# Kernel optimization log

Hardware: AMD Instinct MI355X
Metric: run time of the kernel (lower is better)

The kernel has to match this reference:

```python
import jax, jax.numpy as jnp
import numpy as np

BN_EPS = 1e-5
B, N1, N2, C = 4, 16384, 4096, 128
MLP = [256, 256]
IN_CH = 3 * C


def setup_inputs() -> dict:
    key = jax.random.key(0)
    ks = jax.random.split(key, 32)
    inp = {
        "xyz1": jax.random.normal(ks[0], (B, N1, 3), dtype=jnp.float32),
        "xyz2": jax.random.normal(ks[1], (B, N2, 3), dtype=jnp.float32),
        "points2": jax.random.normal(ks[2], (B, C, N2), dtype=jnp.float32),
        "points1": jax.random.normal(ks[3], (B, C, N1), dtype=jnp.float32),
        "points_b1": jax.random.normal(ks[4], (B, C, N1), dtype=jnp.float32),
    }
    ch = IN_CH
    k = 5
    for i, oc in enumerate(MLP):
        inp[f"w{i}"] = jax.random.normal(ks[k], (oc, ch), dtype=jnp.float32) / np.float32(np.sqrt(ch)); k += 1
        inp[f"b{i}"] = jnp.zeros((oc,), dtype=jnp.float32)
        inp[f"g{i}"] = jax.random.uniform(ks[k], (oc,), minval=0.5, maxval=1.5, dtype=jnp.float32); k += 1
        inp[f"beta{i}"] = 0.1 * jax.random.normal(ks[k], (oc,), dtype=jnp.float32); k += 1
        inp[f"m{i}"] = 0.1 * jax.random.normal(ks[k], (oc,), dtype=jnp.float32); k += 1
        inp[f"v{i}"] = jax.random.uniform(ks[k], (oc,), minval=0.5, maxval=1.5, dtype=jnp.float32); k += 1
        ch = oc
    return inp


def _conv_bn_relu(x, w, b, g, beta, m, v):
    # 1x1 conv over channel dim: x (B, Cin, N) -> (B, Cout, N), BN in eval mode, ReLU
    y = jnp.einsum("oc,bcn->bon", w, x) + b[None, :, None]
    y = (y - m[None, :, None]) * jax.lax.rsqrt(v[None, :, None] + BN_EPS) * g[None, :, None] + beta[None, :, None]
    return jax.nn.relu(y)


def reference(xyz1, xyz2, points2, points1, points_b1,
              w0, b0, g0, beta0, m0, v0,
              w1, b1, g1, beta1, m1, v1):
    # squared pairwise distances (B, N1, N2) via GEMM form
    d = (jnp.sum(xyz1 * xyz1, axis=-1)[:, :, None]
         + jnp.sum(xyz2 * xyz2, axis=-1)[:, None, :]
         - 2.0 * jnp.einsum("bnd,bmd->bnm", xyz1, xyz2))
    neg_d3, idx3 = jax.lax.top_k(-d, 3)              # 3 smallest distances
    d3 = -neg_d3                                      # (B, N1, 3)
    w = 1.0 / d3
    w = w / jnp.sum(w, axis=-1, keepdims=True)        # (B, N1, 3)
    p2t = jnp.transpose(points2, (0, 2, 1))           # (B, N2, C)
    gathered = jax.vmap(lambda p, i: p[i])(p2t, idx3) # (B, N1, 3, C)
    fused = jnp.einsum("bnk,bnkc->bcn", w, gathered)  # (B, C, N1)
    x = jnp.concatenate([points1, fused, points_b1], axis=1)  # (B, 3C, N1)
    x = _conv_bn_relu(x, w0, b0, g0, beta0, m0, v0)
    x = _conv_bn_relu(x, w1, b1, g1, beta1, m1, v1)
    return jnp.max(x, axis=1)                         # (B, N1)
```

## Files before the change

### kernel.cpp

```cpp
#include <hip/hip_runtime.h>

#define N1 16384
#define N2 4096
#define CC 128
#define KIN 384
#define HID 256

typedef unsigned short u16;
typedef unsigned int u32;

typedef _Float16 v8h __attribute__((ext_vector_type(8)));
typedef float v4f __attribute__((ext_vector_type(4)));


__device__ __forceinline__ u16 f2h(float f) {
    _Float16 h = (_Float16)f;
    return __builtin_bit_cast(u16, h);
}

__global__ __launch_bounds__(256) void prep_transpose_kernel(
    const float* __restrict__ w0, const float* __restrict__ w1,
    const float* __restrict__ b0, const float* __restrict__ g0, const float* __restrict__ be0,
    const float* __restrict__ m0, const float* __restrict__ v0,
    const float* __restrict__ b1, const float* __restrict__ g1, const float* __restrict__ be1,
    const float* __restrict__ m1, const float* __restrict__ v1,
    const float* __restrict__ xyz2, const float* __restrict__ points2,
    u16* __restrict__ W0h, u16* __restrict__ W1h,
    float* __restrict__ sst, float4* __restrict__ xyz2q,
    float* __restrict__ p2t)
{
    __shared__ float tile[64][129];
    int tid = threadIdx.x;

    if (blockIdx.x < 256) {
        int bid = blockIdx.x;
        int n20 = (bid & 63) * 64;
        int b   = bid >> 6;

        int jr = tid & 63, cr = tid >> 6;
#pragma unroll 8
        for (int it = 0; it < 32; ++it) {
            int ch = it * 4 + cr;
            tile[jr][ch] = points2[((size_t)b * CC + ch) * N2 + n20 + jr];
        }
        __syncthreads();

        int cw = tid & 127, jw0 = tid >> 7;
#pragma unroll 8
        for (int it = 0; it < 32; ++it) {
            int j = it * 2 + jw0;
            p2t[((size_t)b * N2 + n20 + j) * CC + cw] = tile[j][cw];
        }
        return;
    }

    int id = (blockIdx.x - 256) * 256 + tid;
    if (id < 98304) {
        W0h[id] = f2h(w0[id]);
    } else if (id < 163840) {
        int t = id - 98304;
        W1h[t] = f2h(w1[t]);
    } else if (id < 164352) {
        int t = id - 163840;
        int o = t & 255;
        if (t < 256) {
            float s = g0[o] * rsqrtf(v0[o] + 1e-5f);
            sst[o]       = s;
            sst[256 + o] = (b0[o] - m0[o]) * s + be0[o];
        } else {
            float s = g1[o] * rsqrtf(v1[o] + 1e-5f);
            sst[512 + o] = s;
            sst[768 + o] = (b1[o] - m1[o]) * s + be1[o];
        }
    } else if (id < 180736) {
        int t = id - 164352;
        float x = xyz2[(size_t)t * 3 + 0];
        float y = xyz2[(size_t)t * 3 + 1];
        float z = xyz2[(size_t)t * 3 + 2];
        xyz2q[t] = make_float4(x, y, z, fmaf(x, x, fmaf(y, y, z * z)));
    }
}

#define BINS(t, cand, D0, D1, D2, I0, I1, I2) do {                    \
    bool c0 = (t) < (D0);                                             \
    bool c1 = (t) < (D1);                                             \
    bool c2 = (t) < (D2);                                             \
    I2 = c1 ? (I1) : (c2 ? (cand) : (I2));                \
    I1 = c0 ? (I0) : (c1 ? (cand) : (I1));                \
    I0 = c0 ? (cand) : (I0);                                          \
    D2 = __builtin_amdgcn_fmed3f((D1), (t), (D2));        \
    D1 = __builtin_amdgcn_fmed3f((D0), (t), (D1));        \
    D0 = fminf((t), (D0));                                            \
} while (0)

#define INS3LEX(t, j, D0, D1, D2, I0, I1, I2) do {                    \
    bool lt2 = (t) < (D2) || ((t) == (D2) && (j) < (I2));             \
    bool lt1 = (t) < (D1) || ((t) == (D1) && (j) < (I1));             \
    bool lt0 = (t) < (D0) || ((t) == (D0) && (j) < (I0));             \
    if (lt2) {                                                        \
        if (lt1) {                                                    \
            D2 = (D1); I2 = (I1);                                     \
            if (lt0) { D1 = (D0); I1 = (I0); D0 = (t); I0 = (j); }    \
            else     { D1 = (t); I1 = (j); }                          \
        } else { D2 = (t); I2 = (j); }                                \
    }                                                                 \
} while (0)

#define MERGE_STEP(st, D0, D1, D2, I0, I1, I2) do {                   \
    float e0 = __shfl_xor((D0), (st), 64);                            \
    float e1 = __shfl_xor((D1), (st), 64);                            \
    float e2 = __shfl_xor((D2), (st), 64);                            \
    int   j0 = __shfl_xor((I0), (st), 64);                            \
    int   j1 = __shfl_xor((I1), (st), 64);                            \
    int   j2 = __shfl_xor((I2), (st), 64);                            \
    INS3LEX(e0, j0, D0, D1, D2, I0, I1, I2);                          \
    INS3LEX(e1, j1, D0, D1, D2, I0, I1, I2);                          \
    INS3LEX(e2, j2, D0, D1, D2, I0, I1, I2);                          \
} while (0)

#define KNN_OUT(Q, D0, D1, D2, I0, I1, I2, PP) do {                   \
    float r0 = 1.f / ((D0) + (PP));                                   \
    float r1 = 1.f / ((D1) + (PP));                                   \
    float r2 = 1.f / ((D2) + (PP));                                   \
    float inv = 1.f / (r0 + r1 + r2);                                 \
    size_t o3 = ((size_t)b * N1 + p0 + (Q)) * 3;                      \
    idx3[o3]     = (I0);                                              \
    idx3[o3 + 1] = (I1);                                              \
    idx3[o3 + 2] = (I2);                                              \
    w3[o3]     = r0 * inv;                                            \
    w3[o3 + 1] = r1 * inv;                                            \
    w3[o3 + 2] = r2 * inv;                                            \
} while (0)

__global__ __launch_bounds__(256)
__attribute__((amdgpu_waves_per_eu(8, 8)))
void knn_kernel(
    const float* __restrict__ xyz1, const float4* __restrict__ xyz2q,
    int* __restrict__ idx3, float* __restrict__ w3)
{
    __shared__ float4 slds[1024];

    int tid = threadIdx.x;
    int b   = blockIdx.y;
    int n0  = blockIdx.x * 32;

    int s  = tid & 15;
    int g  = tid >> 4;
    int p0 = n0 + g * 2;

    size_t pb = ((size_t)b * N1 + p0) * 3;
    float x0 = xyz1[pb + 0], y0 = xyz1[pb + 1], z0 = xyz1[pb + 2];
    float x1 = xyz1[pb + 3], y1 = xyz1[pb + 4], z1 = xyz1[pb + 5];
    float ax0 = -2.f * x0, ay0 = -2.f * y0, az0 = -2.f * z0;
    float ax1 = -2.f * x1, ay1 = -2.f * y1, az1 = -2.f * z1;
    float pp0 = fmaf(x0, x0, fmaf(y0, y0, z0 * z0));
    float pp1 = fmaf(x1, x1, fmaf(y1, y1, z1 * z1));

    float da0 = 1e30f, da1 = 1e30f, da2 = 1e30f;
    float db0 = 1e30f, db1 = 1e30f, db2 = 1e30f;
    int   ia0 = 0, ia1 = 0, ia2 = 0;
    int   ib0 = 0, ib1 = 0, ib2 = 0;

#pragma unroll
    for (int stage = 0; stage < 4; ++stage) {
        int base = stage * 1024;
#pragma unroll
        for (int i = 0; i < 4; ++i)
            slds[tid + i * 256] = xyz2q[(size_t)b * N2 + base + tid + i * 256];
        __syncthreads();

#pragma unroll 4
        for (int k = 0; k < 64; ++k) {
            int c = s + (k << 4);
            float4 v = slds[c];
            int cand = base + c;
            float t0 = fmaf(ax0, v.x, fmaf(ay0, v.y, fmaf(az0, v.z, v.w)));
            float t1 = fmaf(ax1, v.x, fmaf(ay1, v.y, fmaf(az1, v.z, v.w)));
            BINS(t0, cand, da0, da1, da2, ia0, ia1, ia2);
            BINS(t1, cand, db0, db1, db2, ib0, ib1, ib2);
        }
        __syncthreads();
    }

#pragma unroll
    for (int st = 1; st <= 8; st <<= 1) {
        MERGE_STEP(st, da0, da1, da2, ia0, ia1, ia2);
        MERGE_STEP(st, db0, db1, db2, ib0, ib1, ib2);
    }

    if (s == 0) {
        KNN_OUT(0, da0, da1, da2, ia0, ia1, ia2, pp0);
        KNN_OUT(1, db0, db1, db2, ib0, ib1, ib2, pp1);
    }
}

__global__ __launch_bounds__(256)
__attribute__((amdgpu_waves_per_eu(5, 5)))
void mlp_kernel(
    const float* __restrict__ points1, const float* __restrict__ pointsb1,
    const float4* __restrict__ p2t4,
    const int* __restrict__ idx3, const float* __restrict__ w3,
    const uint4* __restrict__ W0v, const uint4* __restrict__ W1v,
    const float* __restrict__ sst, float* __restrict__ out)
{
    __shared__ __align__(16) u16 sx[32 * KIN];
    __shared__ float sred[4][32];
    __shared__ int   s_idx[96];
    __shared__ float s_w[96];

    int tid = threadIdx.x;
    int b   = blockIdx.y;
    int n0  = blockIdx.x * 32;

    if (tid < 96) {
        size_t gi = ((size_t)b * N1 + n0) * 3 + tid;
        s_idx[tid] = idx3[gi];
        s_w[tid]   = w3[gi];
    }

    int pL = tid & 31;
    int t4 = (tid >> 5) * 4;
#pragma unroll
    for (int k = 0; k < 4; ++k) {
        int r4 = t4 + 32 * k;
        size_t base = ((size_t)b * CC + r4) * N1 + n0 + pL;
        float a0 = points1[base];
        float a1 = points1[base + (size_t)N1];
        float a2 = points1[base + (size_t)2 * N1];
        float a3 = points1[base + (size_t)3 * N1];
        u32 lo = f2h(a0) | ((u32)f2h(a1) << 16);
        u32 hi = f2h(a2) | ((u32)f2h(a3) << 16);
        int chunk = (r4 >> 3) ^ (pL & 7);
        *(uint2*)&sx[pL * KIN + chunk * 8 + (r4 & 7)] = make_uint2(lo, hi);
    }
#pragma unroll
    for (int k = 0; k < 4; ++k) {
        int r4 = t4 + 32 * k;
        int k4 = 256 + r4;
        size_t base = ((size_t)b * CC + r4) * N1 + n0 + pL;
        float a0 = pointsb1[base];
        float a1 = pointsb1[base + (size_t)N1];
        float a2 = pointsb1[base + (size_t)2 * N1];
        float a3 = pointsb1[base + (size_t)3 * N1];
        u32 lo = f2h(a0) | ((u32)f2h(a1) << 16);
        u32 hi = f2h(a2) | ((u32)f2h(a3) << 16);
        int chunk = (k4 >> 3) ^ (pL & 7);
        *(uint2*)&sx[pL * KIN + chunk * 8 + (k4 & 7)] = make_uint2(lo, hi);
    }
    __syncthreads();

    int c4  = tid & 31;
    int pg  = tid >> 5;
    int k4g = 128 + c4 * 4;
#pragma unroll
    for (int k = 0; k < 4; ++k) {
        int p = pg + 8 * k;
        float w0w = s_w[p * 3 + 0], w1w = s_w[p * 3 + 1], w2w = s_w[p * 3 + 2];
        float4 f0 = p2t4[((size_t)b * N2 + s_idx[p * 3 + 0]) * 32 + c4];
        float4 f1 = p2t4[((size_t)b * N2 + s_idx[p * 3 + 1]) * 32 + c4];
        float4 f2 = p2t4[((size_t)b * N2 + s_idx[p * 3 + 2]) * 32 + c4];
        float e0 = fmaf(w0w, f0.x, fmaf(w1w, f1.x, w2w * f2.x));
        float e1 = fmaf(w0w, f0.y, fmaf(w1w, f1.y, w2w * f2.y));
        float e2 = fmaf(w0w, f0.z, fmaf(w1w, f1.z, w2w * f2.z));
        float e3 = fmaf(w0w, f0.w, fmaf(w1w, f1.w, w2w * f2.w));
        u32 lo = f2h(e0) | ((u32)f2h(e1) << 16);
        u32 hi = f2h(e2) | ((u32)f2h(e3) << 16);
        int chunk = (k4g >> 3) ^ (p & 7);
        *(uint2*)&sx[p * KIN + chunk * 8 + (k4g & 7)] = make_uint2(lo, hi);
    }
    __syncthreads();

    int lane = tid & 63, w = tid >> 6;
    int ml = lane & 15, ql = lane >> 4;
    int px7 = ml & 7;

    v4f acc1[4][2];
#pragma unroll
    for (int ot = 0; ot < 4; ++ot)
        for (int pt = 0; pt < 2; ++pt)
            acc1[ot][pt] = (v4f){0.f, 0.f, 0.f, 0.f};

#pragma unroll
    for (int s = 0; s < 12; ++s) {
        int kc = s * 4 + ql;
        int pc = (kc ^ px7) * 8;
        v8h bf0 = __builtin_bit_cast(v8h, *(const uint4*)&sx[ml * KIN + pc]);
        v8h bf1 = __builtin_bit_cast(v8h, *(const uint4*)&sx[(16 + ml) * KIN + pc]);
#pragma unroll
        for (int ot = 0; ot < 4; ++ot) {
            int o = w * 64 + ot * 16 + ml;
            v8h af = __builtin_bit_cast(v8h, W0v[o * 48 + kc]);
            acc1[ot][0] = __builtin_amdgcn_mfma_f32_16x16x32_f16(af, bf0, acc1[ot][0], 0, 0, 0);
            acc1[ot][1] = __builtin_amdgcn_mfma_f32_16x16x32_f16(af, bf1, acc1[ot][1], 0, 0, 0);
        }
    }
    __syncthreads();

    const float* s0v = sst;
    const float* t0v = sst + 256;
#pragma unroll
    for (int ot = 0; ot < 4; ++ot) {
        int o0 = w * 64 + ot * 16 + ql * 4;
        float sc0 = s0v[o0], sc1 = s0v[o0 + 1], sc2 = s0v[o0 + 2], sc3 = s0v[o0 + 3];
        float sh0 = t0v[o0], sh1 = t0v[o0 + 1], sh2 = t0v[o0 + 2], sh3 = t0v[o0 + 3];
        int chunk = ((o0 >> 3) ^ px7);
#pragma unroll
        for (int pt = 0; pt < 2; ++pt) {
            int p = pt * 16 + ml;
            float z0 = fmaxf(fmaf(acc1[ot][pt][0], sc0, sh0), 0.f);
            float z1 = fmaxf(fmaf(acc1[ot][pt][1], sc1, sh1), 0.f);
            float z2 = fmaxf(fmaf(acc1[ot][pt][2], sc2, sh2), 0.f);
            float z3 = fmaxf(fmaf(acc1[ot][pt][3], sc3, sh3), 0.f);
            u32 lo = f2h(z0) | ((u32)f2h(z1) << 16);
            u32 hi = f2h(z2) | ((u32)f2h(z3) << 16);
            *(uint2*)&sx[p * HID + chunk * 8 + (o0 & 7)] = make_uint2(lo, hi);
        }
    }
    __syncthreads();

    v4f acc2[4][2];
#pragma unroll
    for (int ot = 0; ot < 4; ++ot)
        for (int pt = 0; pt < 2; ++pt)
            acc2[ot][pt] = (v4f){0.f, 0.f, 0.f, 0.f};

#pragma unroll
    for (int s = 0; s < 8; ++s) {
        int kc = s * 4 + ql;
        int pc = (kc ^ px7) * 8;
        v8h bf0 = __builtin_bit_cast(v8h, *(const uint4*)&sx[ml * HID + pc]);
        v8h bf1 = __builtin_bit_cast(v8h, *(const uint4*)&sx[(16 + ml) * HID + pc]);
#pragma unroll
        for (int ot = 0; ot < 4; ++ot) {
            int o = w * 64 + ot * 16 + ml;
            v8h af = __builtin_bit_cast(v8h, W1v[o * 32 + kc]);
            acc2[ot][0] = __builtin_amdgcn_mfma_f32_16x16x32_f16(af, bf0, acc2[ot][0], 0, 0, 0);
            acc2[ot][1] = __builtin_amdgcn_mfma_f32_16x16x32_f16(af, bf1, acc2[ot][1], 0, 0, 0);
        }
    }

    const float* s1v = sst + 512;
    const float* t1v = sst + 768;
    float mx0 = 0.f, mx1 = 0.f;
#pragma unroll
    for (int ot = 0; ot < 4; ++ot) {
        int o0 = w * 64 + ot * 16 + ql * 4;
#pragma unroll
        for (int r = 0; r < 4; ++r) {
            float sc = s1v[o0 + r], sh = t1v[o0 + r];
            mx0 = fmaxf(mx0, fmaf(acc2[ot][0][r], sc, sh));
            mx1 = fmaxf(mx1, fmaf(acc2[ot][1][r], sc, sh));
        }
    }
    mx0 = fmaxf(mx0, __shfl_xor(mx0, 16, 64));
    mx0 = fmaxf(mx0, __shfl_xor(mx0, 32, 64));
    mx1 = fmaxf(mx1, __shfl_xor(mx1, 16, 64));
    mx1 = fmaxf(mx1, __shfl_xor(mx1, 32, 64));
    if (lane < 16) {
        sred[w][ml]      = mx0;
        sred[w][16 + ml] = mx1;
    }
    __syncthreads();
    if (tid < 32)
        out[(size_t)b * N1 + n0 + tid] =
            fmaxf(fmaxf(sred[0][tid], sred[1][tid]),
                  fmaxf(sred[2][tid], sred[3][tid]));
}

extern "C" void kernel_launch(void* const* d_in, const int* in_sizes, int n_in,
                              void* d_out, int out_size, void* d_ws, size_t ws_size,
                              hipStream_t stream)
{
    const float* xyz1     = (const float*)d_in[0];
    const float* xyz2     = (const float*)d_in[1];
    const float* points2  = (const float*)d_in[2];
    const float* points1  = (const float*)d_in[3];
    const float* pointsb1 = (const float*)d_in[4];
    const float* w0   = (const float*)d_in[5];
    const float* b0   = (const float*)d_in[6];
    const float* g0   = (const float*)d_in[7];
    const float* be0  = (const float*)d_in[8];
    const float* m0   = (const float*)d_in[9];
    const float* v0   = (const float*)d_in[10];
    const float* w1   = (const float*)d_in[11];
    const float* b1   = (const float*)d_in[12];
    const float* g1   = (const float*)d_in[13];
    const float* be1  = (const float*)d_in[14];
    const float* m1   = (const float*)d_in[15];
    const float* v1   = (const float*)d_in[16];
    float* out = (float*)d_out;

    char* ws = (char*)d_ws;
    u16*    W0h   = (u16*)(ws + 0);
    u16*    W1h   = (u16*)(ws + 196608);
    float*  sst   = (float*)(ws + 327680);
    float4* xyz2q = (float4*)(ws + 331776);
    int*    idx3  = (int*)(ws + 593920);
    float*  w3    = (float*)(ws + 1380352);
    float*  p2t   = (float*)(ws + 2166784);

    prep_transpose_kernel<<<962, 256, 0, stream>>>(
        w0, w1, b0, g0, be0, m0, v0,
        b1, g1, be1, m1, v1,
        xyz2, points2,
        W0h, W1h, sst, xyz2q, p2t);
    knn_kernel<<<dim3(512, 4), 256, 0, stream>>>(xyz1, xyz2q, idx3, w3);
    mlp_kernel<<<dim3(512, 4), 256, 0, stream>>>(points1, pointsb1,
                                                 (const float4*)p2t, idx3, w3,
                                                 (const uint4*)W0h, (const uint4*)W1h,
                                                 sst, out);
}
```

Before: 316.9 us.

## Retile MLP kernel to 64 points per 512-thread block with 8 waves

The MLP kernel now processes 64 points per block using 512 threads (8 waves). Each wave covers 32 output channels across 4 point tiles instead of 64 channels across 2 tiles. This halves the number of blocks and means each weight fragment loaded from global memory feeds four MFMAs instead of two, cutting weight traffic per point. In exchange, LDS use per block doubles to about 48KB, which may limit occupancy, and the fixed waves_per_eu hint is replaced by launch bounds.

After: 279.2 us, median of 2. 11.9% less time.

```diff
diff --git a/kernel.cpp b/kernel.cpp
--- a/kernel.cpp
+++ b/kernel.cpp
@@ -194,8 +194,7 @@
     }
 }
 
-__global__ __launch_bounds__(256)
-__attribute__((amdgpu_waves_per_eu(5, 5)))
+__global__ __launch_bounds__(512, 4)
 void mlp_kernel(
     const float* __restrict__ points1, const float* __restrict__ pointsb1,
     const float4* __restrict__ p2t4,
@@ -203,26 +202,26 @@
     const uint4* __restrict__ W0v, const uint4* __restrict__ W1v,
     const float* __restrict__ sst, float* __restrict__ out)
 {
-    __shared__ __align__(16) u16 sx[32 * KIN];
-    __shared__ float sred[4][32];
-    __shared__ int   s_idx[96];
-    __shared__ float s_w[96];
+    __shared__ __align__(16) u16 sx[64 * KIN];
+    __shared__ float sred[8][64];
+    __shared__ int   s_idx[192];
+    __shared__ float s_w[192];
 
     int tid = threadIdx.x;
     int b   = blockIdx.y;
-    int n0  = blockIdx.x * 32;
-
-    if (tid < 96) {
+    int n0  = blockIdx.x * 64;
+
+    if (tid < 192) {
         size_t gi = ((size_t)b * N1 + n0) * 3 + tid;
         s_idx[tid] = idx3[gi];
         s_w[tid]   = w3[gi];
     }
 
-    int pL = tid & 31;
-    int t4 = (tid >> 5) * 4;
+    int pL  = tid & 63;
+    int cg4 = (tid >> 6) * 4;
 #pragma unroll
     for (int k = 0; k < 4; ++k) {
-        int r4 = t4 + 32 * k;
+        int r4 = cg4 + 32 * k;
         size_t base = ((size_t)b * CC + r4) * N1 + n0 + pL;
         float a0 = points1[base];
         float a1 = points1[base + (size_t)N1];
@@ -235,7 +234,7 @@
     }
 #pragma unroll
     for (int k = 0; k < 4; ++k) {
-        int r4 = t4 + 32 * k;
+        int r4 = cg4 + 32 * k;
         int k4 = 256 + r4;
         size_t base = ((size_t)b * CC + r4) * N1 + n0 + pL;
         float a0 = pointsb1[base];
@@ -254,7 +253,7 @@
     int k4g = 128 + c4 * 4;
 #pragma unroll
     for (int k = 0; k < 4; ++k) {
-        int p = pg + 8 * k;
+        int p = pg + 16 * k;
         float w0w = s_w[p * 3 + 0], w1w = s_w[p * 3 + 1], w2w = s_w[p * 3 + 2];
         float4 f0 = p2t4[((size_t)b * N2 + s_idx[p * 3 + 0]) * 32 + c4];
         float4 f1 = p2t4[((size_t)b * N2 + s_idx[p * 3 + 1]) * 32 + c4];
@@ -274,10 +273,10 @@
     int ml = lane & 15, ql = lane >> 4;
     int px7 = ml & 7;
 
-    v4f acc1[4][2];
-#pragma unroll
-    for (int ot = 0; ot < 4; ++ot)
-        for (int pt = 0; pt < 2; ++pt)
+    v4f acc1[2][4];
+#pragma unroll
+    for (int ot = 0; ot < 2; ++ot)
+        for (int pt = 0; pt < 4; ++pt)
             acc1[ot][pt] = (v4f){0.f, 0.f, 0.f, 0.f};
 
 #pragma unroll
@@ -286,12 +285,16 @@
         int pc = (kc ^ px7) * 8;
         v8h bf0 = __builtin_bit_cast(v8h, *(const uint4*)&sx[ml * KIN + pc]);
         v8h bf1 = __builtin_bit_cast(v8h, *(const uint4*)&sx[(16 + ml) * KIN + pc]);
-#pragma unroll
-        for (int ot = 0; ot < 4; ++ot) {
-            int o = w * 64 + ot * 16 + ml;
+        v8h bf2 = __builtin_bit_cast(v8h, *(const uint4*)&sx[(32 + ml) * KIN + pc]);
+        v8h bf3 = __builtin_bit_cast(v8h, *(const uint4*)&sx[(48 + ml) * KIN + pc]);
+#pragma unroll
+        for (int ot = 0; ot < 2; ++ot) {
+            int o = w * 32 + ot * 16 + ml;
             v8h af = __builtin_bit_cast(v8h, W0v[o * 48 + kc]);
             acc1[ot][0] = __builtin_amdgcn_mfma_f32_16x16x32_f16(af, bf0, acc1[ot][0], 0, 0, 0);
             acc1[ot][1] = __builtin_amdgcn_mfma_f32_16x16x32_f16(af, bf1, acc1[ot][1], 0, 0, 0);
+            acc1[ot][2] = __builtin_amdgcn_mfma_f32_16x16x32_f16(af, bf2, acc1[ot][2], 0, 0, 0);
+            acc1[ot][3] = __builtin_amdgcn_mfma_f32_16x16x32_f16(af, bf3, acc1[ot][3], 0, 0, 0);
         }
     }
     __syncthreads();
@@ -299,13 +302,13 @@
     const float* s0v = sst;
     const float* t0v = sst + 256;
 #pragma unroll
-    for (int ot = 0; ot < 4; ++ot) {
-        int o0 = w * 64 + ot * 16 + ql * 4;
+    for (int ot = 0; ot < 2; ++ot) {
+        int o0 = w * 32 + ot * 16 + ql * 4;
         float sc0 = s0v[o0], sc1 = s0v[o0 + 1], sc2 = s0v[o0 + 2], sc3 = s0v[o0 + 3];
         float sh0 = t0v[o0], sh1 = t0v[o0 + 1], sh2 = t0v[o0 + 2], sh3 = t0v[o0 + 3];
         int chunk = ((o0 >> 3) ^ px7);
 #pragma unroll
-        for (int pt = 0; pt < 2; ++pt) {
+        for (int pt = 0; pt < 4; ++pt) {
             int p = pt * 16 + ml;
             float z0 = fmaxf(fmaf(acc1[ot][pt][0], sc0, sh0), 0.f);
             float z1 = fmaxf(fmaf(acc1[ot][pt][1], sc1, sh1), 0.f);
@@ -318,10 +321,10 @@
     }
     __syncthreads();
 
-    v4f acc2[4][2];
-#pragma unroll
-    for (int ot = 0; ot < 4; ++ot)
-        for (int pt = 0; pt < 2; ++pt)
+    v4f acc2[2][4];
+#pragma unroll
+    for (int ot = 0; ot < 2; ++ot)
+        for (int pt = 0; pt < 4; ++pt)
             acc2[ot][pt] = (v4f){0.f, 0.f, 0.f, 0.f};
 
 #pragma unroll
@@ -330,41 +333,56 @@
         int pc = (kc ^ px7) * 8;
         v8h bf0 = __builtin_bit_cast(v8h, *(const uint4*)&sx[ml * HID + pc]);
         v8h bf1 = __builtin_bit_cast(v8h, *(const uint4*)&sx[(16 + ml) * HID + pc]);
-#pragma unroll
-        for (int ot = 0; ot < 4; ++ot) {
-            int o = w * 64 + ot * 16 + ml;
+        v8h bf2 = __builtin_bit_cast(v8h, *(const uint4*)&sx[(32 + ml) * HID + pc]);
+        v8h bf3 = __builtin_bit_cast(v8h, *(const uint4*)&sx[(48 + ml) * HID + pc]);
+#pragma unroll
+        for (int ot = 0; ot < 2; ++ot) {
+            int o = w * 32 + ot * 16 + ml;
             v8h af = __builtin_bit_cast(v8h, W1v[o * 32 + kc]);
             acc2[ot][0] = __builtin_amdgcn_mfma_f32_16x16x32_f16(af, bf0, acc2[ot][0], 0, 0, 0);
             acc2[ot][1] = __builtin_amdgcn_mfma_f32_16x16x32_f16(af, bf1, acc2[ot][1], 0, 0, 0);
+            acc2[ot][2] = __builtin_amdgcn_mfma_f32_16x16x32_f16(af, bf2, acc2[ot][2], 0, 0, 0);
+            acc2[ot][3] = __builtin_amdgcn_mfma_f32_16x16x32_f16(af, bf3, acc2[ot][3], 0, 0, 0);
         }
     }
 
     const float* s1v = sst + 512;
     const float* t1v = sst + 768;
-    float mx0 = 0.f, mx1 = 0.f;
-#pragma unroll
-    for (int ot = 0; ot < 4; ++ot) {
-        int o0 = w * 64 + ot * 16 + ql * 4;
+    float mx0 = 0.f, mx1 = 0.f, mx2 = 0.f, mx3 = 0.f;
+#pragma unroll
+    for (int ot = 0; ot < 2; ++ot) {
+        int o0 = w * 32 + ot * 16 + ql * 4;
 #pragma unroll
         for (int r = 0; r < 4; ++r) {
             float sc = s1v[o0 + r], sh = t1v[o0 + r];
             mx0 = fmaxf(mx0, fmaf(acc2[ot][0][r], sc, sh));
             mx1 = fmaxf(mx1, fmaf(acc2[ot][1][r], sc, sh));
+            mx2 = fmaxf(mx2, fmaf(acc2[ot][2][r], sc, sh));
+            mx3 = fmaxf(mx3, fmaf(acc2[ot][3][r], sc, sh));
         }
     }
     mx0 = fmaxf(mx0, __shfl_xor(mx0, 16, 64));
     mx0 = fmaxf(mx0, __shfl_xor(mx0, 32, 64));
     mx1 = fmaxf(mx1, __shfl_xor(mx1, 16, 64));
     mx1 = fmaxf(mx1, __shfl_xor(mx1, 32, 64));
+    mx2 = fmaxf(mx2, __shfl_xor(mx2, 16, 64));
+    mx2 = fmaxf(mx2, __shfl_xor(mx2, 32, 64));
+    mx3 = fmaxf(mx3, __shfl_xor(mx3, 16, 64));
+    mx3 = fmaxf(mx3, __shfl_xor(mx3, 32, 64));
     if (lane < 16) {
         sred[w][ml]      = mx0;
         sred[w][16 + ml] = mx1;
+        sred[w][32 + ml] = mx2;
+        sred[w][48 + ml] = mx3;
     }
     __syncthreads();
-    if (tid < 32)
-        out[(size_t)b * N1 + n0 + tid] =
-            fmaxf(fmaxf(sred[0][tid], sred[1][tid]),
-                  fmaxf(sred[2][tid], sred[3][tid]));
+    if (tid < 64) {
+        float m = sred[0][tid];
+#pragma unroll
+        for (int wv = 1; wv < 8; ++wv)
+            m = fmaxf(m, sred[wv][tid]);
+        out[(size_t)b * N1 + n0 + tid] = m;
+    }
 }
 
 extern "C" void kernel_launch(void* const* d_in, const int* in_sizes, int n_in,
@@ -405,7 +423,7 @@
         xyz2, points2,
         W0h, W1h, sst, xyz2q, p2t);
     knn_kernel<<<dim3(512, 4), 256, 0, stream>>>(xyz1, xyz2q, idx3, w3);
-    mlp_kernel<<<dim3(512, 4), 256, 0, stream>>>(points1, pointsb1,
+    mlp_kernel<<<dim3(256, 4), 512, 0, stream>>>(points1, pointsb1,
                                                  (const float4*)p2t, idx3, w3,
                                                  (const uint4*)W0h, (const uint4*)W1h,
                                                  sst, out);
```
